# Kernel tuning notes

Hardware: AMD Instinct MI355X
Metric: run time of the kernel (lower is better)

The kernel has to match this reference:

```python
import jax, jax.numpy as jnp
import numpy as np

B, A, T, NMODE, H = 4, 16, 32, 8, 256
NSCENE = 512
HEADS = 8
FF = 128
LN_EPS = 1e-6

def _layer_norm(x, g, b, eps=LN_EPS):
    mu = jnp.mean(x, axis=-1, keepdims=True)
    var = jnp.mean((x - mu) ** 2, axis=-1, keepdims=True)
    return (x - mu) * jax.lax.rsqrt(var + eps) * g + b


def setup_inputs() -> dict:
    key = jax.random.key(0)
    ks = jax.random.split(key, 16)
    s = 1.0 / np.sqrt(H)
    sf = 1.0 / np.sqrt(FF)
    return {
        "hidden_vecs": jax.random.normal(ks[0], (B, A, T, NMODE, H), jnp.float32),
        "scene_hidden_vec": jax.random.normal(ks[1], (B, NSCENE, H), jnp.float32),
        # nn.MultiheadAttention packed in_proj: rows [Wq; Wk; Wv]
        "in_proj_w": jax.random.normal(ks[2], (3 * H, H), jnp.float32) * s,
        "in_proj_b": jnp.zeros((3 * H,), jnp.float32),
        "out_proj_w": jax.random.normal(ks[3], (H, H), jnp.float32) * s,
        "out_proj_b": jnp.zeros((H,), jnp.float32),
        "attn_ln_g": jnp.ones((H,), jnp.float32),
        "attn_ln_b": jnp.zeros((H,), jnp.float32),
        "ff1_w": jax.random.normal(ks[4], (FF, H), jnp.float32) * s,
        "ff1_b": jnp.zeros((FF,), jnp.float32),
        "ff2_w": jax.random.normal(ks[5], (H, FF), jnp.float32) * sf,
        "ff2_b": jnp.zeros((H,), jnp.float32),
        "ff_ln_g": jnp.ones((H,), jnp.float32),
        "ff_ln_b": jnp.zeros((H,), jnp.float32),
    }


def reference(hidden_vecs, scene_hidden_vec, in_proj_w, in_proj_b, out_proj_w,
              out_proj_b, attn_ln_g, attn_ln_b, ff1_w, ff1_b, ff2_w, ff2_b,
              ff_ln_g, ff_ln_b):
    b, a, t, n, h = hidden_vecs.shape
    N = scene_hidden_vec.shape[1]
    d = h // HEADS
    m = a * t * n  # queries per batch element

    Wq, Wk, Wv = in_proj_w[:h], in_proj_w[h:2 * h], in_proj_w[2 * h:]
    bq, bk, bv = in_proj_b[:h], in_proj_b[h:2 * h], in_proj_b[2 * h:]

    # Project queries; K/V computed ONCE per batch (shared across a,t,n) --
    # avoids materializing the (b,a,t,n,N,h) expanded tensor.
    q = (hidden_vecs.reshape(b, m, h) @ Wq.T + bq).reshape(b, m, HEADS, d)
    k = (scene_hidden_vec @ Wk.T + bk).reshape(b, N, HEADS, d)
    v = (scene_hidden_vec @ Wv.T + bv).reshape(b, N, HEADS, d)

    scale = 1.0 / np.sqrt(d)
    scores = jnp.einsum('bmed,bned->bemn', q * scale, k)  # (b, heads, m, N)
    attn = jax.nn.softmax(scores, axis=-1)
    ctx = jnp.einsum('bemn,bned->bmed', attn, v).reshape(b, m, h)
    attn_out = (ctx @ out_proj_w.T + out_proj_b).reshape(b, a, t, n, h)

    # averaged attention weights over heads (average_attn_weights=True)
    attn_score = jnp.mean(attn, axis=1).reshape(b, a, t, n, 1, N)

    x = _layer_norm(attn_out + hidden_vecs, attn_ln_g, attn_ln_b)
    ff = jax.nn.relu(x @ ff1_w.T + ff1_b) @ ff2_w.T + ff2_b
    out = _layer_norm(ff + x, ff_ln_g, ff_ln_b)
    return out, attn_score
```

## Files before the change

kernel.cpp:

```cpp
#include <hip/hip_runtime.h>
#include <hip/hip_bf16.h>

#define H 256
#define NSC 512
#define MQ 4096
#define BATCH 4

typedef __attribute__((ext_vector_type(8))) short bf16x8;
typedef __attribute__((ext_vector_type(4))) float f32x4;

__device__ __forceinline__ ushort f2bf(float x) {
    union { float f; unsigned u; } c; c.f = x;
    unsigned r = c.u + 0x7FFF + ((c.u >> 16) & 1);
    return (ushort)(r >> 16);
}
__device__ __forceinline__ unsigned pk2(float hi, float lo) {
    union { float f; unsigned u; } a, b; a.f = hi; b.f = lo;
    return __builtin_amdgcn_perm(a.u, b.u, 0x07060302u);
}
__device__ __forceinline__ uint4 cvt8f(const float* p) {
    float4 a = *(const float4*)p;
    float4 b = *(const float4*)(p + 4);
    uint4 r;
    r.x = pk2(a.y, a.x); r.y = pk2(a.w, a.z);
    r.z = pk2(b.y, b.x); r.w = pk2(b.w, b.z);
    return r;
}
#define EXP2(x) __builtin_amdgcn_exp2f(x)

template<int MODE>
__device__ __forceinline__ void gemm_body(
    ushort* As, ushort* Bs, int bx, int by,
    const float* __restrict__ Ain, const float* __restrict__ W,
    const float* __restrict__ bias,
    void* __restrict__ out, ushort* __restrict__ out2,
    int K, int N, float alpha)
{
    const int t = threadIdx.x;
    const int w = t >> 6, lane = t & 63, g = lane >> 4, l15 = lane & 15;
    const int rowBase = by * 64;
    const int colBase = bx * 256;
    const int wr = (w >> 2) * 32;
    const int wc = (w & 3) * 64;
    f32x4 acc[2][4];
    #pragma unroll
    for (int mt = 0; mt < 2; mt++)
        #pragma unroll
        for (int nt = 0; nt < 4; nt++) acc[mt][nt] = (f32x4){0.f,0.f,0.f,0.f};

    const int sr = t >> 3, skc = t & 7, sp = skc ^ (sr & 7);
    const size_t arow = (size_t)(rowBase + sr) * K + skc * 8;

    uint4 av = cvt8f(Ain + arow);
    uint4 bv[4];
    #pragma unroll
    for (int i = 0; i < 4; i++) {
        const int u = t + 512*i, br = u >> 3, bkc = u & 7;
        int brow = colBase + br; if (brow > N - 1) brow = N - 1;
        bv[i] = cvt8f(W + (size_t)brow * K + bkc*8);
    }

    for (int k0 = 0; k0 < K; k0 += 64) {
        __syncthreads();
        *(uint4*)&As[sr*64 + sp*8] = av;
        #pragma unroll
        for (int i = 0; i < 4; i++) {
            const int u = t + 512*i, br = u >> 3, bkc = u & 7, bp = bkc ^ (br & 7);
            *(uint4*)&Bs[br*64 + bp*8] = bv[i];
        }
        __syncthreads();
        if (k0 + 64 < K) {
            av = cvt8f(Ain + arow + k0 + 64);
            #pragma unroll
            for (int i = 0; i < 4; i++) {
                const int u = t + 512*i, br = u >> 3, bkc = u & 7;
                int brow = colBase + br; if (brow > N - 1) brow = N - 1;
                bv[i] = cvt8f(W + (size_t)brow * K + k0 + 64 + bkc*8);
            }
        }
        #pragma unroll
        for (int kk = 0; kk < 2; kk++) {
            const int swz = ((kk*4 + g) ^ (l15 & 7)) * 8;
            bf16x8 af[2], bfr[4];
            #pragma unroll
            for (int mt = 0; mt < 2; mt++)
                af[mt] = *(const bf16x8*)&As[(wr + mt*16 + l15)*64 + swz];
            #pragma unroll
            for (int nt = 0; nt < 4; nt++)
                bfr[nt] = *(const bf16x8*)&Bs[(wc + nt*16 + l15)*64 + swz];
            #pragma unroll
            for (int mt = 0; mt < 2; mt++)
                #pragma unroll
                for (int nt = 0; nt < 4; nt++)
                    acc[mt][nt] = __builtin_amdgcn_mfma_f32_16x16x32_bf16(
                        af[mt], bfr[nt], acc[mt][nt], 0, 0, 0);
        }
    }

    #pragma unroll
    for (int nt = 0; nt < 4; nt++) {
        const int col = colBase + wc + nt*16 + l15;
        const float bb = bias[col];
        #pragma unroll
        for (int mt = 0; mt < 2; mt++) {
            const int row0 = rowBase + wr + mt*16 + g*4;
            if (col < 256) {
                #pragma unroll
                for (int r = 0; r < 4; r++)
                    ((ushort*)out)[(size_t)(row0 + r) * 256 + col] = f2bf(acc[mt][nt][r] + bb);
            } else {
                ushort4 pkv = { f2bf(acc[mt][nt][0] + bb), f2bf(acc[mt][nt][1] + bb),
                                f2bf(acc[mt][nt][2] + bb), f2bf(acc[mt][nt][3] + bb) };
                *(ushort4*)&out2[(size_t)((row0 >> 9)*256 + col - 256) * 512 + (row0 & 511)] = pkv;
            }
        }
    }
}

__global__ __launch_bounds__(512, 4) void kv_kernel(
    const float* __restrict__ scene,
    const float* __restrict__ in_w, const float* __restrict__ in_b,
    ushort* __restrict__ kb, ushort* __restrict__ vtb)
{
    __shared__ ushort As[64 * 64];
    __shared__ ushort Bs[256 * 64];
    gemm_body<1>(As, Bs, blockIdx.x >> 5, blockIdx.x & 31,
                 scene, in_w + 65536, in_b + 256, kb, vtb, 256, 512, 1.f);
}

__global__ __launch_bounds__(1024, 4) void mega_kernel(
    const float* __restrict__ hidden,
    const float* __restrict__ Wq, const float* __restrict__ bq,
    const ushort* __restrict__ k, const ushort* __restrict__ vt,
    const float* __restrict__ Wo, const float* __restrict__ bo,
    const float* __restrict__ ag, const float* __restrict__ ab,
    const float* __restrict__ W1, const float* __restrict__ b1,
    const float* __restrict__ W2, const float* __restrict__ b2,
    const float* __restrict__ fg, const float* __restrict__ fbv,
    float* __restrict__ out, float* __restrict__ attn_score,
    float alpha_q)
{
    __shared__ uint4 SHraw[9120];
    ushort* SH = (ushort*)SHraw;
    ushort* Ks  = SH;
    ushort* Vs  = SH + 8448;
    ushort* Pb  = SH + 18688;
    ushort* As0 = SH;
    ushort* Bs0 = SH + 4096;
    ushort* Bs  = SH;
    ushort* Xb  = SH + 16384;
    float*  Ls  = (float*)(SH + 32768);
    float*  Lq  = (float*)(SH + 33280);
    ushort* Qb  = SH + 39168;
    ushort* Fb  = SH + 39168;
    ushort* Cb  = SH + 55552;
    float*  Lg  = (float*)(SH + 71936);

    const int t = threadIdx.x;
    const int w = t >> 6, lane = t & 63, g = lane >> 4, l15 = lane & 15;
    const int b = blockIdx.x >> 6;
    const int m0 = (blockIdx.x & 63) * 64;
    const size_t rowG = (size_t)b * MQ + m0;
    const size_t kg = (size_t)b * NSC * H;
    const size_t vg = (size_t)b * H * NSC;

    const int wr = (w >> 2) * 16;
    const int wc = (w & 3) * 64;

    {
        f32x4 acc[4];
        #pragma unroll
        for (int nt = 0; nt < 4; nt++) acc[nt] = (f32x4){0.f,0.f,0.f,0.f};

        const int sr = t >> 3, skc = t & 7, sp = skc ^ (sr & 7);
        uint4 av;
        if (t < 512) av = cvt8f(hidden + (rowG + sr) * 256 + skc*8);
        uint4 bv[2];
        #pragma unroll
        for (int i = 0; i < 2; i++) {
            const int u = t + 1024*i, br = u >> 3, bkc = u & 7;
            bv[i] = cvt8f(Wq + (size_t)br * 256 + bkc*8);
        }
        for (int k0 = 0; k0 < 256; k0 += 64) {
            __syncthreads();
            if (t < 512) *(uint4*)&As0[sr*64 + sp*8] = av;
            #pragma unroll
            for (int i = 0; i < 2; i++) {
                const int u = t + 1024*i, br = u >> 3, bkc = u & 7, bp = bkc ^ (br & 7);
                *(uint4*)&Bs0[br*64 + bp*8] = bv[i];
            }
            __syncthreads();
            if (k0 < 192) {
                if (t < 512) av = cvt8f(hidden + (rowG + sr) * 256 + k0 + 64 + skc*8);
                #pragma unroll
                for (int i = 0; i < 2; i++) {
                    const int u = t + 1024*i, br = u >> 3, bkc = u & 7;
                    bv[i] = cvt8f(Wq + (size_t)br * 256 + k0 + 64 + bkc*8);
                }
            }
            #pragma unroll
            for (int kk = 0; kk < 2; kk++) {
                const int swz = ((kk*4 + g) ^ (l15 & 7)) * 8;
                bf16x8 af = *(const bf16x8*)&As0[(wr + l15)*64 + swz];
                #pragma unroll
                for (int nt = 0; nt < 4; nt++) {
                    bf16x8 bfr = *(const bf16x8*)&Bs0[(wc + nt*16 + l15)*64 + swz];
                    acc[nt] = __builtin_amdgcn_mfma_f32_16x16x32_bf16(
                        af, bfr, acc[nt], 0, 0, 0);
                }
            }
        }
        #pragma unroll
        for (int nt = 0; nt < 4; nt++) {
            const int col = wc + nt*16 + l15;
            const float bb = bq[col];
            #pragma unroll
            for (int r = 0; r < 4; r++) {
                const int qr = wr + g*4 + r;
                const float o = (acc[nt][r] + bb) * alpha_q;
                Qb[qr*256 + (((col >> 3) ^ (qr & 7)) << 3) + (col & 7)] = f2bf(o);
            }
        }
    }
    __syncthreads();

    const int hh0 = w & 7, hf = w >> 3;
    bf16x8 qf[2];
    #pragma unroll
    for (int qt = 0; qt < 2; qt++) {
        const int qr0 = hf*32 + qt*16 + l15;
        const int c0 = hh0*32 + g*8;
        qf[qt] = *(const bf16x8*)&Qb[qr0*256 + (((c0 >> 3) ^ (qr0 & 7)) << 3)];
    }

    f32x4 cacc[2][2];
    float lacc[2][4];
    #pragma unroll
    for (int qt = 0; qt < 2; qt++) {
        #pragma unroll
        for (int dt = 0; dt < 2; dt++) cacc[qt][dt] = (f32x4){0.f,0.f,0.f,0.f};
        #pragma unroll
        for (int r = 0; r < 4; r++) lacc[qt][r] = 0.f;
    }

    const int skey = t >> 5, spart = t & 31;
    const int sd = t >> 2, sp2 = t & 3;
    bf16x8 kr = *(const bf16x8*)&k[kg + (size_t)skey*H + spart*8];
    bf16x8 vr = *(const bf16x8*)&vt[vg + (size_t)sd*NSC + sp2*8];

    for (int c = 0; c < 16; c++) {
        const int kbase = c * 32;
        __syncthreads();
        *(bf16x8*)&Ks[skey*264 + spart*8] = kr;
        *(bf16x8*)&Vs[sd*40 + sp2*8] = vr;
        __syncthreads();
        if (c < 15) {
            kr = *(const bf16x8*)&k[kg + (size_t)(kbase + 32 + skey)*H + spart*8];
            vr = *(const bf16x8*)&vt[vg + (size_t)sd*NSC + kbase + 32 + sp2*8];
        }
        #pragma unroll
        for (int qt = 0; qt < 2; qt++) {
            #pragma unroll
            for (int kt = 0; kt < 2; kt++) {
                bf16x8 kf = *(const bf16x8*)&Ks[(kt*16 + l15)*264 + hh0*32 + g*8];
                f32x4 s = __builtin_amdgcn_mfma_f32_16x16x32_bf16(
                    qf[qt], kf, (f32x4){0.f,0.f,0.f,0.f}, 0, 0, 0);
                #pragma unroll
                for (int r = 0; r < 4; r++) {
                    float p = EXP2(s[r]);
                    lacc[qt][r] += p;
                    Pb[(w*32 + qt*16 + g*4 + r)*40 + kt*16 + l15] = f2bf(p);
                }
            }
        }
        #pragma unroll
        for (int qt = 0; qt < 2; qt++) {
            bf16x8 pf = *(const bf16x8*)&Pb[(w*32 + qt*16 + l15)*40 + g*8];
            #pragma unroll
            for (int dt = 0; dt < 2; dt++) {
                bf16x8 vf = *(const bf16x8*)&Vs[(hh0*32 + dt*16 + l15)*40 + g*8];
                cacc[qt][dt] = __builtin_amdgcn_mfma_f32_16x16x32_bf16(
                    pf, vf, cacc[qt][dt], 0, 0, 0);
            }
        }
    }

    #pragma unroll
    for (int qt = 0; qt < 2; qt++) {
        float invl[4];
        #pragma unroll
        for (int r = 0; r < 4; r++) {
            float v = lacc[qt][r];
            v += __shfl_xor(v, 1); v += __shfl_xor(v, 2);
            v += __shfl_xor(v, 4); v += __shfl_xor(v, 8);
            invl[r] = 1.f / v;
            if (l15 == 0) Lg[hh0*64 + hf*32 + qt*16 + g*4 + r] = -__log2f(v) - 3.0f;
        }
        #pragma unroll
        for (int dt = 0; dt < 2; dt++)
            #pragma unroll
            for (int r = 0; r < 4; r++) {
                const int qr = hf*32 + qt*16 + g*4 + r;
                const int col = hh0*32 + dt*16 + l15;
                Cb[qr*256 + (((col >> 3) ^ (qr & 7)) << 3) + (col & 7)]
                    = f2bf(cacc[qt][dt][r] * invl[r]);
            }
    }

    __syncthreads();

    {
        f32x4 sacc[4][2];
        #pragma unroll
        for (int qt = 0; qt < 4; qt++)
            #pragma unroll
            for (int kt = 0; kt < 2; kt++) sacc[qt][kt] = (f32x4){0.f,0.f,0.f,0.f};

        #pragma unroll 2
        for (int h = 0; h < 8; h++) {
            float lgq[4]; bf16x8 qv[4];
            #pragma unroll
            for (int qt = 0; qt < 4; qt++) {
                lgq[qt] = Lg[h*64 + qt*16 + l15];
                const int qr0 = qt*16 + l15;
                const int c0 = h*32 + g*8;
                qv[qt] = *(const bf16x8*)&Qb[qr0*256 + (((c0 >> 3) ^ (qr0 & 7)) << 3)];
            }
            #pragma unroll
            for (int kt = 0; kt < 2; kt++) {
                bf16x8 kf2 = *(const bf16x8*)&k[kg + (size_t)(w*32 + kt*16 + l15)*H + h*32 + g*8];
                #pragma unroll
                for (int qt = 0; qt < 4; qt++) {
                    f32x4 s = __builtin_amdgcn_mfma_f32_16x16x32_bf16(
                        kf2, qv[qt], (f32x4){0.f,0.f,0.f,0.f}, 0, 0, 0);
                    #pragma unroll
                    for (int r = 0; r < 4; r++) sacc[qt][kt][r] += EXP2(s[r] + lgq[qt]);
                }
            }
        }
        #pragma unroll
        for (int qt = 0; qt < 4; qt++)
            #pragma unroll
            for (int kt = 0; kt < 2; kt++)
                *(f32x4*)&attn_score[(rowG + qt*16 + l15)*NSC + w*32 + kt*16 + g*4]
                    = sacc[qt][kt];
    }

    float xres[4][4];
    {
        f32x4 acc[4];
        #pragma unroll
        for (int nt = 0; nt < 4; nt++) acc[nt] = (f32x4){0.f,0.f,0.f,0.f};

        uint4 bv[2];
        #pragma unroll
        for (int i = 0; i < 2; i++) {
            const int u = t + 1024*i, br = u >> 3, bkc = u & 7;
            bv[i] = cvt8f(Wo + (size_t)br * 256 + bkc*8);
        }
        for (int k0 = 0; k0 < 256; k0 += 64) {
            __syncthreads();
            #pragma unroll
            for (int i = 0; i < 2; i++) {
                const int u = t + 1024*i, br = u >> 3, bkc = u & 7, bp = bkc ^ (br & 7);
                *(uint4*)&Bs[br*64 + bp*8] = bv[i];
            }
            __syncthreads();
            if (k0 < 192) {
                #pragma unroll
                for (int i = 0; i < 2; i++) {
                    const int u = t + 1024*i, br = u >> 3, bkc = u & 7;
                    bv[i] = cvt8f(Wo + (size_t)br * 256 + k0 + 64 + bkc*8);
                }
            }
            #pragma unroll
            for (int kk = 0; kk < 2; kk++) {
                const int rowC = wr + l15;
                const int gi = (k0 >> 3) + kk*4 + g;
                bf16x8 af = *(const bf16x8*)&Cb[rowC*256 + ((gi ^ (rowC & 7)) << 3)];
                const int swz = ((kk*4 + g) ^ (l15 & 7)) * 8;
                #pragma unroll
                for (int nt = 0; nt < 4; nt++) {
                    bf16x8 bfr = *(const bf16x8*)&Bs[(wc + nt*16 + l15)*64 + swz];
                    acc[nt] = __builtin_amdgcn_mfma_f32_16x16x32_bf16(
                        af, bfr, acc[nt], 0, 0, 0);
                }
            }
        }
        float bb[4], gmv[4], btv[4];
        #pragma unroll
        for (int nt = 0; nt < 4; nt++) {
            const int col = wc + nt*16 + l15;
            bb[nt] = bo[col]; gmv[nt] = ag[col]; btv[nt] = ab[col];
        }
        #pragma unroll
        for (int r = 0; r < 4; r++) {
            const float* rp = hidden + (rowG + wr + g*4 + r) * 256;
            #pragma unroll
            for (int nt = 0; nt < 4; nt++)
                acc[nt][r] += bb[nt] + rp[wc + nt*16 + l15];
        }
        float ps[4], pq[4];
        #pragma unroll
        for (int r = 0; r < 4; r++) {
            float s = (acc[0][r] + acc[1][r]) + (acc[2][r] + acc[3][r]);
            float qq = (acc[0][r]*acc[0][r] + acc[1][r]*acc[1][r])
                     + (acc[2][r]*acc[2][r] + acc[3][r]*acc[3][r]);
            #pragma unroll
            for (int m = 1; m < 16; m <<= 1) {
                s += __shfl_xor(s, m);
                qq += __shfl_xor(qq, m);
            }
            ps[r] = s; pq[r] = qq;
        }
        if (l15 == 0) {
            #pragma unroll
            for (int r = 0; r < 4; r++) {
                const int ri = wr + g*4 + r;
                Ls[ri*4 + (w & 3)] = ps[r];
                Lq[ri*4 + (w & 3)] = pq[r];
            }
        }
        __syncthreads();
        #pragma unroll
        for (int r = 0; r < 4; r++) {
            const int ri = wr + g*4 + r;
            f32x4 sv = *(const f32x4*)&Ls[ri*4];
            f32x4 qv2 = *(const f32x4*)&Lq[ri*4];
            const float mu = (sv[0]+sv[1]+sv[2]+sv[3]) * (1.f/256.f);
            const float ex2 = (qv2[0]+qv2[1]+qv2[2]+qv2[3]) * (1.f/256.f);
            const float rs = rsqrtf(ex2 - mu*mu + 1e-6f);
            #pragma unroll
            for (int nt = 0; nt < 4; nt++) {
                const int col = wc + nt*16 + l15;
                const float o = (acc[nt][r] - mu) * rs * gmv[nt] + btv[nt];
                xres[nt][r] = o;
                Xb[ri*256 + (((col >> 3) ^ (ri & 7)) << 3) + (col & 7)] = f2bf(o);
            }
        }
    }

    {
        const int wrB = (w >> 2) * 16;
        const int wcB = (w & 3) * 32;
        f32x4 facc[2];
        #pragma unroll
        for (int nt = 0; nt < 2; nt++) facc[nt] = (f32x4){0.f,0.f,0.f,0.f};

        uint4 bv2 = cvt8f(W1 + (size_t)(t >> 3) * 256 + (t & 7)*8);
        for (int k0 = 0; k0 < 256; k0 += 64) {
            __syncthreads();
            {
                const int br = t >> 3, bkc = t & 7, bp = bkc ^ (br & 7);
                *(uint4*)&Bs[br*64 + bp*8] = bv2;
            }
            __syncthreads();
            if (k0 < 192)
                bv2 = cvt8f(W1 + (size_t)(t >> 3) * 256 + k0 + 64 + (t & 7)*8);
            #pragma unroll
            for (int kk = 0; kk < 2; kk++) {
                const int rowX = wrB + l15;
                const int gi = (k0 >> 3) + kk*4 + g;
                bf16x8 af = *(const bf16x8*)&Xb[rowX*256 + ((gi ^ (rowX & 7)) << 3)];
                const int swz = ((kk*4 + g) ^ (l15 & 7)) * 8;
                #pragma unroll
                for (int nt = 0; nt < 2; nt++) {
                    bf16x8 bfr = *(const bf16x8*)&Bs[(wcB + nt*16 + l15)*64 + swz];
                    facc[nt] = __builtin_amdgcn_mfma_f32_16x16x32_bf16(
                        af, bfr, facc[nt], 0, 0, 0);
                }
            }
        }
        __syncthreads();
        #pragma unroll
        for (int nt = 0; nt < 2; nt++) {
            const int colF = wcB + nt*16 + l15;
            const float fbb = b1[colF];
            #pragma unroll
            for (int r = 0; r < 4; r++) {
                const int rowF = wrB + g*4 + r;
                const float o = fmaxf(facc[nt][r] + fbb, 0.f);
                Fb[rowF*128 + (((colF >> 3) ^ (rowF & 7)) << 3) + (colF & 7)] = f2bf(o);
            }
        }
        __syncthreads();
    }

    {
        f32x4 acc2[4];
        #pragma unroll
        for (int nt = 0; nt < 4; nt++) acc2[nt] = (f32x4){0.f,0.f,0.f,0.f};

        uint4 bv3[2];
        #pragma unroll
        for (int i = 0; i < 2; i++) {
            const int u = t + 1024*i, br = u >> 3, bkc = u & 7;
            bv3[i] = cvt8f(W2 + (size_t)br * 128 + bkc*8);
        }
        for (int k0 = 0; k0 < 128; k0 += 64) {
            __syncthreads();
            #pragma unroll
            for (int i = 0; i < 2; i++) {
                const int u = t + 1024*i, br = u >> 3, bkc = u & 7, bp = bkc ^ (br & 7);
                *(uint4*)&Bs[br*64 + bp*8] = bv3[i];
            }
            __syncthreads();
            if (k0 == 0) {
                #pragma unroll
                for (int i = 0; i < 2; i++) {
                    const int u = t + 1024*i, br = u >> 3, bkc = u & 7;
                    bv3[i] = cvt8f(W2 + (size_t)br * 128 + 64 + bkc*8);
                }
            }
            #pragma unroll
            for (int kk = 0; kk < 2; kk++) {
                const int gi = (k0 >> 3) + kk*4 + g;
                const int rowF = wr + l15;
                bf16x8 af2 = *(const bf16x8*)&Fb[rowF*128 + ((gi ^ (rowF & 7)) << 3)];
                const int swz = ((kk*4 + g) ^ (l15 & 7)) * 8;
                #pragma unroll
                for (int nt = 0; nt < 4; nt++) {
                    bf16x8 bfr = *(const bf16x8*)&Bs[(wc + nt*16 + l15)*64 + swz];
                    acc2[nt] = __builtin_amdgcn_mfma_f32_16x16x32_bf16(
                        af2, bfr, acc2[nt], 0, 0, 0);
                }
            }
        }
        float bb[4], gmv[4], btv[4];
        #pragma unroll
        for (int nt = 0; nt < 4; nt++) {
            const int col = wc + nt*16 + l15;
            bb[nt] = b2[col]; gmv[nt] = fg[col]; btv[nt] = fbv[col];
        }
        #pragma unroll
        for (int r = 0; r < 4; r++)
            #pragma unroll
            for (int nt = 0; nt < 4; nt++)
                acc2[nt][r] += bb[nt] + xres[nt][r];
        float ps[4], pq[4];
        #pragma unroll
        for (int r = 0; r < 4; r++) {
            float s = (acc2[0][r] + acc2[1][r]) + (acc2[2][r] + acc2[3][r]);
            float qq = (acc2[0][r]*acc2[0][r] + acc2[1][r]*acc2[1][r])
                     + (acc2[2][r]*acc2[2][r] + acc2[3][r]*acc2[3][r]);
            #pragma unroll
            for (int m = 1; m < 16; m <<= 1) {
                s += __shfl_xor(s, m);
                qq += __shfl_xor(qq, m);
            }
            ps[r] = s; pq[r] = qq;
        }
        __syncthreads();
        if (l15 == 0) {
            #pragma unroll
            for (int r = 0; r < 4; r++) {
                const int ri = wr + g*4 + r;
                Ls[ri*4 + (w & 3)] = ps[r];
                Lq[ri*4 + (w & 3)] = pq[r];
            }
        }
        __syncthreads();
        #pragma unroll
        for (int r = 0; r < 4; r++) {
            const int ri = wr + g*4 + r;
            f32x4 sv = *(const f32x4*)&Ls[ri*4];
            f32x4 qv2 = *(const f32x4*)&Lq[ri*4];
            const float mu = (sv[0]+sv[1]+sv[2]+sv[3]) * (1.f/256.f);
            const float ex2 = (qv2[0]+qv2[1]+qv2[2]+qv2[3]) * (1.f/256.f);
            const float rs = rsqrtf(ex2 - mu*mu + 1e-6f);
            #pragma unroll
            for (int nt = 0; nt < 4; nt++) {
                const int col = wc + nt*16 + l15;
                out[(rowG + ri) * 256 + col] =
                    (acc2[nt][r] - mu) * rs * gmv[nt] + btv[nt];
            }
        }
    }
}

extern "C" void kernel_launch(void* const* d_in, const int* in_sizes, int n_in,
                              void* d_out, int out_size, void* d_ws, size_t ws_size,
                              hipStream_t stream)
{
    const float* hidden = (const float*)d_in[0];
    const float* scene  = (const float*)d_in[1];
    const float* in_w   = (const float*)d_in[2];
    const float* in_b   = (const float*)d_in[3];
    const float* out_w  = (const float*)d_in[4];
    const float* out_b  = (const float*)d_in[5];
    const float* aln_g  = (const float*)d_in[6];
    const float* aln_b  = (const float*)d_in[7];
    const float* ff1_w  = (const float*)d_in[8];
    const float* ff1_b  = (const float*)d_in[9];
    const float* ff2_w  = (const float*)d_in[10];
    const float* ff2_b  = (const float*)d_in[11];
    const float* fln_g  = (const float*)d_in[12];
    const float* fln_b  = (const float*)d_in[13];

    float* out0  = (float*)d_out;
    float* score = out0 + (size_t)BATCH * MQ * H;

    ushort* kb   = (ushort*)d_ws;
    ushort* vtb  = kb + 524288;

    const float alpha_q = 0.25507609683638066f;

    kv_kernel<<<dim3(64), dim3(512), 0, stream>>>(scene, in_w, in_b, kb, vtb);
    mega_kernel<<<dim3(256), dim3(1024), 0, stream>>>(
        hidden, in_w, in_b, kb, vtb,
        out_w, out_b, aln_g, aln_b,
        ff1_w, ff1_b, ff2_w, ff2_b, fln_g, fln_b,
        out0, score, alpha_q);
}
```

Baseline: 167.2 us.

## Halve mega_kernel query tile to 32 rows with 512 threads

Each block of the fused attention+FFN kernel now handles 32 query rows with 8 waves instead of 64 rows with 16 waves, and the grid doubles to 512 blocks. The LDS layout is shrunk and remapped, and each wave now owns one head across all 32 queries. Per-wave P staging is merged into the QK loop, and V fragments are hoisted out of the loop. This is meant to give more blocks than the 256 CUs to fill the GPU and to cut LDS per block for higher occupancy. The cost is that K/V and weight tiles are reloaded twice as many times in total.

```diff
diff --git a/kernel.cpp b/kernel.cpp
--- a/kernel.cpp
+++ b/kernel.cpp
@@ -128,7 +128,7 @@
                  scene, in_w + 65536, in_b + 256, kb, vtb, 256, 512, 1.f);
 }
 
-__global__ __launch_bounds__(1024, 4) void mega_kernel(
+__global__ __launch_bounds__(512, 4) void mega_kernel(
     const float* __restrict__ hidden,
     const float* __restrict__ Wq, const float* __restrict__ bq,
     const ushort* __restrict__ k, const ushort* __restrict__ vt,
@@ -140,26 +140,26 @@
     float* __restrict__ out, float* __restrict__ attn_score,
     float alpha_q)
 {
-    __shared__ uint4 SHraw[9120];
+    __shared__ uint4 SHraw[5088];
     ushort* SH = (ushort*)SHraw;
     ushort* Ks  = SH;
     ushort* Vs  = SH + 8448;
     ushort* Pb  = SH + 18688;
     ushort* As0 = SH;
-    ushort* Bs0 = SH + 4096;
+    ushort* Bs0 = SH + 2048;
     ushort* Bs  = SH;
-    ushort* Xb  = SH + 16384;
-    float*  Ls  = (float*)(SH + 32768);
-    float*  Lq  = (float*)(SH + 33280);
-    ushort* Qb  = SH + 39168;
-    ushort* Fb  = SH + 39168;
-    ushort* Cb  = SH + 55552;
-    float*  Lg  = (float*)(SH + 71936);
+    float*  Ls  = (float*)(SH + 16384);
+    float*  Lq  = (float*)(SH + 16640);
+    ushort* Qb  = SH + 23808;
+    ushort* Xb  = SH + 23808;
+    ushort* Cb  = SH + 32000;
+    ushort* Fb  = SH + 32000;
+    float*  Lg  = (float*)(SH + 40192);
 
     const int t = threadIdx.x;
     const int w = t >> 6, lane = t & 63, g = lane >> 4, l15 = lane & 15;
-    const int b = blockIdx.x >> 6;
-    const int m0 = (blockIdx.x & 63) * 64;
+    const int b = blockIdx.x >> 7;
+    const int m0 = (blockIdx.x & 127) * 32;
     const size_t rowG = (size_t)b * MQ + m0;
     const size_t kg = (size_t)b * NSC * H;
     const size_t vg = (size_t)b * H * NSC;
@@ -174,27 +174,27 @@
 
         const int sr = t >> 3, skc = t & 7, sp = skc ^ (sr & 7);
         uint4 av;
-        if (t < 512) av = cvt8f(hidden + (rowG + sr) * 256 + skc*8);
-        uint4 bv[2];
-        #pragma unroll
-        for (int i = 0; i < 2; i++) {
-            const int u = t + 1024*i, br = u >> 3, bkc = u & 7;
+        if (t < 256) av = cvt8f(hidden + (rowG + sr) * 256 + skc*8);
+        uint4 bv[4];
+        #pragma unroll
+        for (int i = 0; i < 4; i++) {
+            const int u = t + 512*i, br = u >> 3, bkc = u & 7;
             bv[i] = cvt8f(Wq + (size_t)br * 256 + bkc*8);
         }
         for (int k0 = 0; k0 < 256; k0 += 64) {
             __syncthreads();
-            if (t < 512) *(uint4*)&As0[sr*64 + sp*8] = av;
-            #pragma unroll
-            for (int i = 0; i < 2; i++) {
-                const int u = t + 1024*i, br = u >> 3, bkc = u & 7, bp = bkc ^ (br & 7);
+            if (t < 256) *(uint4*)&As0[sr*64 + sp*8] = av;
+            #pragma unroll
+            for (int i = 0; i < 4; i++) {
+                const int u = t + 512*i, br = u >> 3, bkc = u & 7, bp = bkc ^ (br & 7);
                 *(uint4*)&Bs0[br*64 + bp*8] = bv[i];
             }
             __syncthreads();
             if (k0 < 192) {
-                if (t < 512) av = cvt8f(hidden + (rowG + sr) * 256 + k0 + 64 + skc*8);
-                #pragma unroll
-                for (int i = 0; i < 2; i++) {
-                    const int u = t + 1024*i, br = u >> 3, bkc = u & 7;
+                if (t < 256) av = cvt8f(hidden + (rowG + sr) * 256 + k0 + 64 + skc*8);
+                #pragma unroll
+                for (int i = 0; i < 4; i++) {
+                    const int u = t + 512*i, br = u >> 3, bkc = u & 7;
                     bv[i] = cvt8f(Wq + (size_t)br * 256 + k0 + 64 + bkc*8);
                 }
             }
@@ -224,13 +224,11 @@
     }
     __syncthreads();
 
-    const int hh0 = w & 7, hf = w >> 3;
     bf16x8 qf[2];
     #pragma unroll
     for (int qt = 0; qt < 2; qt++) {
-        const int qr0 = hf*32 + qt*16 + l15;
-        const int c0 = hh0*32 + g*8;
-        qf[qt] = *(const bf16x8*)&Qb[qr0*256 + (((c0 >> 3) ^ (qr0 & 7)) << 3)];
+        const int qr0 = qt*16 + l15;
+        qf[qt] = *(const bf16x8*)&Qb[qr0*256 + (((w*4 + g) ^ (qr0 & 7)) << 3)];
     }
 
     f32x4 cacc[2][2];
@@ -243,45 +241,56 @@
         for (int r = 0; r < 4; r++) lacc[qt][r] = 0.f;
     }
 
-    const int skey = t >> 5, spart = t & 31;
-    const int sd = t >> 2, sp2 = t & 3;
-    bf16x8 kr = *(const bf16x8*)&k[kg + (size_t)skey*H + spart*8];
-    bf16x8 vr = *(const bf16x8*)&vt[vg + (size_t)sd*NSC + sp2*8];
+    bf16x8 kr[2], vr[2];
+    #pragma unroll
+    for (int i = 0; i < 2; i++) {
+        const int u = t + 512*i;
+        kr[i] = *(const bf16x8*)&k[kg + (size_t)(u >> 5)*H + (u & 31)*8];
+        vr[i] = *(const bf16x8*)&vt[vg + (size_t)(u >> 2)*NSC + (u & 3)*8];
+    }
+    ushort* PbW = Pb + w*640;
 
     for (int c = 0; c < 16; c++) {
         const int kbase = c * 32;
         __syncthreads();
-        *(bf16x8*)&Ks[skey*264 + spart*8] = kr;
-        *(bf16x8*)&Vs[sd*40 + sp2*8] = vr;
+        #pragma unroll
+        for (int i = 0; i < 2; i++) {
+            const int u = t + 512*i;
+            *(bf16x8*)&Ks[(u >> 5)*264 + (u & 31)*8] = kr[i];
+            *(bf16x8*)&Vs[(u >> 2)*40 + (u & 3)*8] = vr[i];
+        }
         __syncthreads();
         if (c < 15) {
-            kr = *(const bf16x8*)&k[kg + (size_t)(kbase + 32 + skey)*H + spart*8];
-            vr = *(const bf16x8*)&vt[vg + (size_t)sd*NSC + kbase + 32 + sp2*8];
-        }
+            #pragma unroll
+            for (int i = 0; i < 2; i++) {
+                const int u = t + 512*i;
+                kr[i] = *(const bf16x8*)&k[kg + (size_t)(kbase + 32 + (u >> 5))*H + (u & 31)*8];
+                vr[i] = *(const bf16x8*)&vt[vg + (size_t)(u >> 2)*NSC + kbase + 32 + (u & 3)*8];
+            }
+        }
+        bf16x8 vfv[2];
+        #pragma unroll
+        for (int dt = 0; dt < 2; dt++)
+            vfv[dt] = *(const bf16x8*)&Vs[(w*32 + dt*16 + l15)*40 + g*8];
         #pragma unroll
         for (int qt = 0; qt < 2; qt++) {
             #pragma unroll
             for (int kt = 0; kt < 2; kt++) {
-                bf16x8 kf = *(const bf16x8*)&Ks[(kt*16 + l15)*264 + hh0*32 + g*8];
+                bf16x8 kf = *(const bf16x8*)&Ks[(kt*16 + l15)*264 + w*32 + g*8];
                 f32x4 s = __builtin_amdgcn_mfma_f32_16x16x32_bf16(
                     qf[qt], kf, (f32x4){0.f,0.f,0.f,0.f}, 0, 0, 0);
                 #pragma unroll
                 for (int r = 0; r < 4; r++) {
                     float p = EXP2(s[r]);
                     lacc[qt][r] += p;
-                    Pb[(w*32 + qt*16 + g*4 + r)*40 + kt*16 + l15] = f2bf(p);
-                }
-            }
-        }
-        #pragma unroll
-        for (int qt = 0; qt < 2; qt++) {
-            bf16x8 pf = *(const bf16x8*)&Pb[(w*32 + qt*16 + l15)*40 + g*8];
-            #pragma unroll
-            for (int dt = 0; dt < 2; dt++) {
-                bf16x8 vf = *(const bf16x8*)&Vs[(hh0*32 + dt*16 + l15)*40 + g*8];
+                    PbW[(g*4 + r)*40 + kt*16 + l15] = f2bf(p);
+                }
+            }
+            bf16x8 pf = *(const bf16x8*)&PbW[l15*40 + g*8];
+            #pragma unroll
+            for (int dt = 0; dt < 2; dt++)
                 cacc[qt][dt] = __builtin_amdgcn_mfma_f32_16x16x32_bf16(
-                    pf, vf, cacc[qt][dt], 0, 0, 0);
-            }
+                    pf, vfv[dt], cacc[qt][dt], 0, 0, 0);
         }
     }
 
@@ -294,14 +303,14 @@
             v += __shfl_xor(v, 1); v += __shfl_xor(v, 2);
             v += __shfl_xor(v, 4); v += __shfl_xor(v, 8);
             invl[r] = 1.f / v;
-            if (l15 == 0) Lg[hh0*64 + hf*32 + qt*16 + g*4 + r] = -__log2f(v) - 3.0f;
+            if (l15 == 0) Lg[w*32 + qt*16 + g*4 + r] = -__log2f(v) - 3.0f;
         }
         #pragma unroll
         for (int dt = 0; dt < 2; dt++)
             #pragma unroll
             for (int r = 0; r < 4; r++) {
-                const int qr = hf*32 + qt*16 + g*4 + r;
-                const int col = hh0*32 + dt*16 + l15;
+                const int qr = qt*16 + g*4 + r;
+                const int col = w*32 + dt*16 + l15;
                 Cb[qr*256 + (((col >> 3) ^ (qr & 7)) << 3) + (col & 7)]
                     = f2bf(cacc[qt][dt][r] * invl[r]);
             }
@@ -310,39 +319,36 @@
     __syncthreads();
 
     {
-        f32x4 sacc[4][2];
-        #pragma unroll
-        for (int qt = 0; qt < 4; qt++)
-            #pragma unroll
-            for (int kt = 0; kt < 2; kt++) sacc[qt][kt] = (f32x4){0.f,0.f,0.f,0.f};
+        f32x4 sacc[2][4];
+        #pragma unroll
+        for (int qt = 0; qt < 2; qt++)
+            #pragma unroll
+            for (int kt = 0; kt < 4; kt++) sacc[qt][kt] = (f32x4){0.f,0.f,0.f,0.f};
 
         #pragma unroll 2
         for (int h = 0; h < 8; h++) {
-            float lgq[4]; bf16x8 qv[4];
-            #pragma unroll
-            for (int qt = 0; qt < 4; qt++) {
-                lgq[qt] = Lg[h*64 + qt*16 + l15];
-                const int qr0 = qt*16 + l15;
-                const int c0 = h*32 + g*8;
-                qv[qt] = *(const bf16x8*)&Qb[qr0*256 + (((c0 >> 3) ^ (qr0 & 7)) << 3)];
-            }
-            #pragma unroll
-            for (int kt = 0; kt < 2; kt++) {
-                bf16x8 kf2 = *(const bf16x8*)&k[kg + (size_t)(w*32 + kt*16 + l15)*H + h*32 + g*8];
-                #pragma unroll
-                for (int qt = 0; qt < 4; qt++) {
-                    f32x4 s = __builtin_amdgcn_mfma_f32_16x16x32_bf16(
-                        kf2, qv[qt], (f32x4){0.f,0.f,0.f,0.f}, 0, 0, 0);
-                    #pragma unroll
-                    for (int r = 0; r < 4; r++) sacc[qt][kt][r] += EXP2(s[r] + lgq[qt]);
-                }
-            }
-        }
-        #pragma unroll
-        for (int qt = 0; qt < 4; qt++)
-            #pragma unroll
-            for (int kt = 0; kt < 2; kt++)
-                *(f32x4*)&attn_score[(rowG + qt*16 + l15)*NSC + w*32 + kt*16 + g*4]
+            const float lg0 = Lg[h*32 + l15];
+            const float lg1 = Lg[h*32 + 16 + l15];
+            bf16x8 q0 = *(const bf16x8*)&Qb[l15*256 + (((h*4 + g) ^ (l15 & 7)) << 3)];
+            bf16x8 q1 = *(const bf16x8*)&Qb[(16 + l15)*256 + (((h*4 + g) ^ (l15 & 7)) << 3)];
+            #pragma unroll
+            for (int kt = 0; kt < 4; kt++) {
+                bf16x8 kf2 = *(const bf16x8*)&k[kg + (size_t)(w*64 + kt*16 + l15)*H + h*32 + g*8];
+                f32x4 s0 = __builtin_amdgcn_mfma_f32_16x16x32_bf16(
+                    kf2, q0, (f32x4){0.f,0.f,0.f,0.f}, 0, 0, 0);
+                #pragma unroll
+                for (int r = 0; r < 4; r++) sacc[0][kt][r] += EXP2(s0[r] + lg0);
+                f32x4 s1 = __builtin_amdgcn_mfma_f32_16x16x32_bf16(
+                    kf2, q1, (f32x4){0.f,0.f,0.f,0.f}, 0, 0, 0);
+                #pragma unroll
+                for (int r = 0; r < 4; r++) sacc[1][kt][r] += EXP2(s1[r] + lg1);
+            }
+        }
+        #pragma unroll
+        for (int qt = 0; qt < 2; qt++)
+            #pragma unroll
+            for (int kt = 0; kt < 4; kt++)
+                *(f32x4*)&attn_score[(rowG + qt*16 + l15)*NSC + w*64 + kt*16 + g*4]
                     = sacc[qt][kt];
     }
 
@@ -352,24 +358,24 @@
         #pragma unroll
         for (int nt = 0; nt < 4; nt++) acc[nt] = (f32x4){0.f,0.f,0.f,0.f};
 
-        uint4 bv[2];
-        #pragma unroll
-        for (int i = 0; i < 2; i++) {
-            const int u = t + 1024*i, br = u >> 3, bkc = u & 7;
+        uint4 bv[4];
+        #pragma unroll
+        for (int i = 0; i < 4; i++) {
+            const int u = t + 512*i, br = u >> 3, bkc = u & 7;
             bv[i] = cvt8f(Wo + (size_t)br * 256 + bkc*8);
         }
         for (int k0 = 0; k0 < 256; k0 += 64) {
             __syncthreads();
             #pragma unroll
-            for (int i = 0; i < 2; i++) {
-                const int u = t + 1024*i, br = u >> 3, bkc = u & 7, bp = bkc ^ (br & 7);
+            for (int i = 0; i < 4; i++) {
+                const int u = t + 512*i, br = u >> 3, bkc = u & 7, bp = bkc ^ (br & 7);
                 *(uint4*)&Bs[br*64 + bp*8] = bv[i];
             }
             __syncthreads();
             if (k0 < 192) {
                 #pragma unroll
-                for (int i = 0; i < 2; i++) {
-                    const int u = t + 1024*i, br = u >> 3, bkc = u & 7;
+                for (int i = 0; i < 4; i++) {
+                    const int u = t + 512*i, br = u >> 3, bkc = u & 7;
                     bv[i] = cvt8f(Wo + (size_t)br * 256 + k0 + 64 + bkc*8);
                 }
             }
@@ -447,16 +453,27 @@
         #pragma unroll
         for (int nt = 0; nt < 2; nt++) facc[nt] = (f32x4){0.f,0.f,0.f,0.f};
 
-        uint4 bv2 = cvt8f(W1 + (size_t)(t >> 3) * 256 + (t & 7)*8);
+        uint4 bv2[2];
+        #pragma unroll
+        for (int i = 0; i < 2; i++) {
+            const int u = t + 512*i, br = u >> 3, bkc = u & 7;
+            bv2[i] = cvt8f(W1 + (size_t)br * 256 + bkc*8);
+        }
         for (int k0 = 0; k0 < 256; k0 += 64) {
             __syncthreads();
-            {
-                const int br = t >> 3, bkc = t & 7, bp = bkc ^ (br & 7);
-                *(uint4*)&Bs[br*64 + bp*8] = bv2;
-            }
-            __syncthreads();
-            if (k0 < 192)
-                bv2 = cvt8f(W1 + (size_t)(t >> 3) * 256 + k0 + 64 + (t & 7)*8);
+            #pragma unroll
+            for (int i = 0; i < 2; i++) {
+                const int u = t + 512*i, br = u >> 3, bkc = u & 7, bp = bkc ^ (br & 7);
+                *(uint4*)&Bs[br*64 + bp*8] = bv2[i];
+            }
+            __syncthreads();
+            if (k0 < 192) {
+                #pragma unroll
+                for (int i = 0; i < 2; i++) {
+                    const int u = t + 512*i, br = u >> 3, bkc = u & 7;
+                    bv2[i] = cvt8f(W1 + (size_t)br * 256 + k0 + 64 + bkc*8);
+                }
+            }
             #pragma unroll
             for (int kk = 0; kk < 2; kk++) {
                 const int rowX = wrB + l15;
@@ -491,24 +508,24 @@
         #pragma unroll
         for (int nt = 0; nt < 4; nt++) acc2[nt] = (f32x4){0.f,0.f,0.f,0.f};
 
-        uint4 bv3[2];
-        #pragma unroll
-        for (int i = 0; i < 2; i++) {
-            const int u = t + 1024*i, br = u >> 3, bkc = u & 7;
+        uint4 bv3[4];
+        #pragma unroll
+        for (int i = 0; i < 4; i++) {
+            const int u = t + 512*i, br = u >> 3, bkc = u & 7;
             bv3[i] = cvt8f(W2 + (size_t)br * 128 + bkc*8);
         }
         for (int k0 = 0; k0 < 128; k0 += 64) {
             __syncthreads();
             #pragma unroll
-            for (int i = 0; i < 2; i++) {
-                const int u = t + 1024*i, br = u >> 3, bkc = u & 7, bp = bkc ^ (br & 7);
+            for (int i = 0; i < 4; i++) {
+                const int u = t + 512*i, br = u >> 3, bkc = u & 7, bp = bkc ^ (br & 7);
                 *(uint4*)&Bs[br*64 + bp*8] = bv3[i];
             }
             __syncthreads();
             if (k0 == 0) {
                 #pragma unroll
-                for (int i = 0; i < 2; i++) {
-                    const int u = t + 1024*i, br = u >> 3, bkc = u & 7;
+                for (int i = 0; i < 4; i++) {
+                    const int u = t + 512*i, br = u >> 3, bkc = u & 7;
                     bv3[i] = cvt8f(W2 + (size_t)br * 128 + 64 + bkc*8);
                 }
             }
@@ -606,7 +623,7 @@
     const float alpha_q = 0.25507609683638066f;
 
     kv_kernel<<<dim3(64), dim3(512), 0, stream>>>(scene, in_w, in_b, kb, vtb);
-    mega_kernel<<<dim3(256), dim3(1024), 0, stream>>>(
+    mega_kernel<<<dim3(512), dim3(512), 0, stream>>>(
         hidden, in_w, in_b, kb, vtb,
         out_w, out_b, aln_g, aln_b,
         ff1_w, ff1_b, ff2_w, ff2_b, fln_g, fln_b,
```

Result: slower. 175.1 us (+4.7%).

## Double K-step tile depth in fused attention and GEMM stages, prefetch K/V early

Applied to the files above, without the earlier changes.

Raises the K-dimension staging chunk from 64 to 128 in the Q-projection, out-projection, FF1 and FF2 GEMMs, and from 32 to 64 keys per attention chunk. This halves the number of barrier-separated load/compute iterations. The shared-memory layout is reorganised, with XOR swizzles replacing the padded strides for K/V. The first K/V chunk is also prefetched before the Q projection so its latency overlaps that GEMM. The cost is more shared memory and more registers per thread, which could lower occupancy or cause spills.

```diff
diff --git a/kernel.cpp b/kernel.cpp
--- a/kernel.cpp
+++ b/kernel.cpp
@@ -140,21 +140,21 @@
     float* __restrict__ out, float* __restrict__ attn_score,
     float alpha_q)
 {
-    __shared__ uint4 SHraw[9120];
+    __shared__ uint4 SHraw[9600];
     ushort* SH = (ushort*)SHraw;
     ushort* Ks  = SH;
-    ushort* Vs  = SH + 8448;
-    ushort* Pb  = SH + 18688;
+    ushort* Vs  = SH + 16384;
+    ushort* Pb  = SH + 32768;
     ushort* As0 = SH;
-    ushort* Bs0 = SH + 4096;
+    ushort* Bs0 = SH + 8192;
     ushort* Bs  = SH;
-    ushort* Xb  = SH + 16384;
     float*  Ls  = (float*)(SH + 32768);
     float*  Lq  = (float*)(SH + 33280);
-    ushort* Qb  = SH + 39168;
-    ushort* Fb  = SH + 39168;
-    ushort* Cb  = SH + 55552;
-    float*  Lg  = (float*)(SH + 71936);
+    ushort* Qb  = SH + 43008;
+    ushort* Xb  = SH + 43008;
+    ushort* Cb  = SH + 59392;
+    ushort* Fb  = SH + 59392;
+    float*  Lg  = (float*)(SH + 75776);
 
     const int t = threadIdx.x;
     const int w = t >> 6, lane = t & 63, g = lane >> 4, l15 = lane & 15;
@@ -167,44 +167,51 @@
     const int wr = (w >> 2) * 16;
     const int wc = (w & 3) * 64;
 
+    bf16x8 kr[2], vr[2];
+    #pragma unroll
+    for (int i = 0; i < 2; i++) {
+        const int u = t + 1024*i;
+        kr[i] = *(const bf16x8*)&k[kg + (size_t)(u >> 5)*H + (u & 31)*8];
+        vr[i] = *(const bf16x8*)&vt[vg + (size_t)(u >> 3)*NSC + (u & 7)*8];
+    }
+
     {
         f32x4 acc[4];
         #pragma unroll
         for (int nt = 0; nt < 4; nt++) acc[nt] = (f32x4){0.f,0.f,0.f,0.f};
 
-        const int sr = t >> 3, skc = t & 7, sp = skc ^ (sr & 7);
-        uint4 av;
-        if (t < 512) av = cvt8f(hidden + (rowG + sr) * 256 + skc*8);
-        uint4 bv[2];
-        #pragma unroll
-        for (int i = 0; i < 2; i++) {
-            const int u = t + 1024*i, br = u >> 3, bkc = u & 7;
-            bv[i] = cvt8f(Wq + (size_t)br * 256 + bkc*8);
-        }
-        for (int k0 = 0; k0 < 256; k0 += 64) {
+        const int ar = t >> 4, agi = t & 15;
+        uint4 av = cvt8f(hidden + (rowG + ar) * 256 + agi*8);
+        uint4 bv[4];
+        #pragma unroll
+        for (int i = 0; i < 4; i++) {
+            const int u = t + 1024*i, br = u >> 4, bgi = u & 15;
+            bv[i] = cvt8f(Wq + (size_t)br * 256 + bgi*8);
+        }
+        for (int k0 = 0; k0 < 256; k0 += 128) {
             __syncthreads();
-            if (t < 512) *(uint4*)&As0[sr*64 + sp*8] = av;
-            #pragma unroll
-            for (int i = 0; i < 2; i++) {
-                const int u = t + 1024*i, br = u >> 3, bkc = u & 7, bp = bkc ^ (br & 7);
-                *(uint4*)&Bs0[br*64 + bp*8] = bv[i];
+            *(uint4*)&As0[ar*128 + ((agi ^ (ar & 7)))*8] = av;
+            #pragma unroll
+            for (int i = 0; i < 4; i++) {
+                const int u = t + 1024*i, br = u >> 4, bgi = u & 15;
+                *(uint4*)&Bs0[br*128 + ((bgi ^ (br & 7)))*8] = bv[i];
             }
             __syncthreads();
-            if (k0 < 192) {
-                if (t < 512) av = cvt8f(hidden + (rowG + sr) * 256 + k0 + 64 + skc*8);
-                #pragma unroll
-                for (int i = 0; i < 2; i++) {
-                    const int u = t + 1024*i, br = u >> 3, bkc = u & 7;
-                    bv[i] = cvt8f(Wq + (size_t)br * 256 + k0 + 64 + bkc*8);
-                }
-            }
-            #pragma unroll
-            for (int kk = 0; kk < 2; kk++) {
+            if (k0 == 0) {
+                av = cvt8f(hidden + (rowG + ar) * 256 + 128 + agi*8);
+                #pragma unroll
+                for (int i = 0; i < 4; i++) {
+                    const int u = t + 1024*i, br = u >> 4, bgi = u & 15;
+                    bv[i] = cvt8f(Wq + (size_t)br * 256 + 128 + bgi*8);
+                }
+            }
+            #pragma unroll
+            for (int kk = 0; kk < 4; kk++) {
                 const int swz = ((kk*4 + g) ^ (l15 & 7)) * 8;
-                bf16x8 af = *(const bf16x8*)&As0[(wr + l15)*64 + swz];
+                bf16x8 af = *(const bf16x8*)&As0[(wr + l15)*128 + swz];
                 #pragma unroll
                 for (int nt = 0; nt < 4; nt++) {
-                    bf16x8 bfr = *(const bf16x8*)&Bs0[(wc + nt*16 + l15)*64 + swz];
+                    bf16x8 bfr = *(const bf16x8*)&Bs0[(wc + nt*16 + l15)*128 + swz];
                     acc[nt] = __builtin_amdgcn_mfma_f32_16x16x32_bf16(
                         af, bfr, acc[nt], 0, 0, 0);
                 }
@@ -229,8 +236,7 @@
     #pragma unroll
     for (int qt = 0; qt < 2; qt++) {
         const int qr0 = hf*32 + qt*16 + l15;
-        const int c0 = hh0*32 + g*8;
-        qf[qt] = *(const bf16x8*)&Qb[qr0*256 + (((c0 >> 3) ^ (qr0 & 7)) << 3)];
+        qf[qt] = *(const bf16x8*)&Qb[qr0*256 + (((hh0*4 + g) ^ (qr0 & 7)) << 3)];
     }
 
     f32x4 cacc[2][2];
@@ -242,45 +248,56 @@
         #pragma unroll
         for (int r = 0; r < 4; r++) lacc[qt][r] = 0.f;
     }
-
-    const int skey = t >> 5, spart = t & 31;
-    const int sd = t >> 2, sp2 = t & 3;
-    bf16x8 kr = *(const bf16x8*)&k[kg + (size_t)skey*H + spart*8];
-    bf16x8 vr = *(const bf16x8*)&vt[vg + (size_t)sd*NSC + sp2*8];
-
-    for (int c = 0; c < 16; c++) {
-        const int kbase = c * 32;
-        __syncthreads();
-        *(bf16x8*)&Ks[skey*264 + spart*8] = kr;
-        *(bf16x8*)&Vs[sd*40 + sp2*8] = vr;
-        __syncthreads();
-        if (c < 15) {
-            kr = *(const bf16x8*)&k[kg + (size_t)(kbase + 32 + skey)*H + spart*8];
-            vr = *(const bf16x8*)&vt[vg + (size_t)sd*NSC + kbase + 32 + sp2*8];
-        }
-        #pragma unroll
-        for (int qt = 0; qt < 2; qt++) {
-            #pragma unroll
-            for (int kt = 0; kt < 2; kt++) {
-                bf16x8 kf = *(const bf16x8*)&Ks[(kt*16 + l15)*264 + hh0*32 + g*8];
-                f32x4 s = __builtin_amdgcn_mfma_f32_16x16x32_bf16(
-                    qf[qt], kf, (f32x4){0.f,0.f,0.f,0.f}, 0, 0, 0);
-                #pragma unroll
-                for (int r = 0; r < 4; r++) {
-                    float p = EXP2(s[r]);
-                    lacc[qt][r] += p;
-                    Pb[(w*32 + qt*16 + g*4 + r)*40 + kt*16 + l15] = f2bf(p);
-                }
-            }
-        }
-        #pragma unroll
-        for (int qt = 0; qt < 2; qt++) {
-            bf16x8 pf = *(const bf16x8*)&Pb[(w*32 + qt*16 + l15)*40 + g*8];
+    ushort* PbW = Pb + w*640;
+
+    for (int c = 0; c < 8; c++) {
+        const int kbase = c * 64;
+        __syncthreads();
+        #pragma unroll
+        for (int i = 0; i < 2; i++) {
+            const int u = t + 1024*i;
+            const int key = u >> 5, gi = u & 31;
+            *(bf16x8*)&Ks[key*256 + ((gi ^ (key & 7)))*8] = kr[i];
+            const int d = u >> 3, gj = u & 7;
+            *(bf16x8*)&Vs[d*64 + ((gj ^ (d & 7)))*8] = vr[i];
+        }
+        __syncthreads();
+        if (c < 7) {
+            #pragma unroll
+            for (int i = 0; i < 2; i++) {
+                const int u = t + 1024*i;
+                kr[i] = *(const bf16x8*)&k[kg + (size_t)(kbase + 64 + (u >> 5))*H + (u & 31)*8];
+                vr[i] = *(const bf16x8*)&vt[vg + (size_t)(u >> 3)*NSC + kbase + 64 + (u & 7)*8];
+            }
+        }
+        #pragma unroll
+        for (int ks2 = 0; ks2 < 2; ks2++) {
+            bf16x8 vfv[2];
             #pragma unroll
             for (int dt = 0; dt < 2; dt++) {
-                bf16x8 vf = *(const bf16x8*)&Vs[(hh0*32 + dt*16 + l15)*40 + g*8];
-                cacc[qt][dt] = __builtin_amdgcn_mfma_f32_16x16x32_bf16(
-                    pf, vf, cacc[qt][dt], 0, 0, 0);
+                const int d = hh0*32 + dt*16 + l15;
+                vfv[dt] = *(const bf16x8*)&Vs[d*64 + (((ks2*4 + g) ^ (l15 & 7)) << 3)];
+            }
+            #pragma unroll
+            for (int qt = 0; qt < 2; qt++) {
+                #pragma unroll
+                for (int kt = 0; kt < 2; kt++) {
+                    const int key = ks2*32 + kt*16 + l15;
+                    bf16x8 kf = *(const bf16x8*)&Ks[key*256 + (((hh0*4 + g) ^ (l15 & 7)) << 3)];
+                    f32x4 s = __builtin_amdgcn_mfma_f32_16x16x32_bf16(
+                        qf[qt], kf, (f32x4){0.f,0.f,0.f,0.f}, 0, 0, 0);
+                    #pragma unroll
+                    for (int r = 0; r < 4; r++) {
+                        float p = EXP2(s[r]);
+                        lacc[qt][r] += p;
+                        PbW[(g*4 + r)*40 + kt*16 + l15] = f2bf(p);
+                    }
+                }
+                bf16x8 pf = *(const bf16x8*)&PbW[l15*40 + g*8];
+                #pragma unroll
+                for (int dt = 0; dt < 2; dt++)
+                    cacc[qt][dt] = __builtin_amdgcn_mfma_f32_16x16x32_bf16(
+                        pf, vfv[dt], cacc[qt][dt], 0, 0, 0);
             }
         }
     }
@@ -323,8 +340,7 @@
             for (int qt = 0; qt < 4; qt++) {
                 lgq[qt] = Lg[h*64 + qt*16 + l15];
                 const int qr0 = qt*16 + l15;
-                const int c0 = h*32 + g*8;
-                qv[qt] = *(const bf16x8*)&Qb[qr0*256 + (((c0 >> 3) ^ (qr0 & 7)) << 3)];
+                qv[qt] = *(const bf16x8*)&Qb[qr0*256 + (((h*4 + g) ^ (qr0 & 7)) << 3)];
             }
             #pragma unroll
             for (int kt = 0; kt < 2; kt++) {
@@ -352,36 +368,36 @@
         #pragma unroll
         for (int nt = 0; nt < 4; nt++) acc[nt] = (f32x4){0.f,0.f,0.f,0.f};
 
-        uint4 bv[2];
-        #pragma unroll
-        for (int i = 0; i < 2; i++) {
-            const int u = t + 1024*i, br = u >> 3, bkc = u & 7;
-            bv[i] = cvt8f(Wo + (size_t)br * 256 + bkc*8);
-        }
-        for (int k0 = 0; k0 < 256; k0 += 64) {
+        uint4 bv[4];
+        #pragma unroll
+        for (int i = 0; i < 4; i++) {
+            const int u = t + 1024*i, br = u >> 4, bgi = u & 15;
+            bv[i] = cvt8f(Wo + (size_t)br * 256 + bgi*8);
+        }
+        for (int k0 = 0; k0 < 256; k0 += 128) {
             __syncthreads();
             #pragma unroll
-            for (int i = 0; i < 2; i++) {
-                const int u = t + 1024*i, br = u >> 3, bkc = u & 7, bp = bkc ^ (br & 7);
-                *(uint4*)&Bs[br*64 + bp*8] = bv[i];
+            for (int i = 0; i < 4; i++) {
+                const int u = t + 1024*i, br = u >> 4, bgi = u & 15;
+                *(uint4*)&Bs[br*128 + ((bgi ^ (br & 7)))*8] = bv[i];
             }
             __syncthreads();
-            if (k0 < 192) {
-                #pragma unroll
-                for (int i = 0; i < 2; i++) {
-                    const int u = t + 1024*i, br = u >> 3, bkc = u & 7;
-                    bv[i] = cvt8f(Wo + (size_t)br * 256 + k0 + 64 + bkc*8);
-                }
-            }
-            #pragma unroll
-            for (int kk = 0; kk < 2; kk++) {
+            if (k0 == 0) {
+                #pragma unroll
+                for (int i = 0; i < 4; i++) {
+                    const int u = t + 1024*i, br = u >> 4, bgi = u & 15;
+                    bv[i] = cvt8f(Wo + (size_t)br * 256 + 128 + bgi*8);
+                }
+            }
+            #pragma unroll
+            for (int kk = 0; kk < 4; kk++) {
                 const int rowC = wr + l15;
                 const int gi = (k0 >> 3) + kk*4 + g;
                 bf16x8 af = *(const bf16x8*)&Cb[rowC*256 + ((gi ^ (rowC & 7)) << 3)];
                 const int swz = ((kk*4 + g) ^ (l15 & 7)) * 8;
                 #pragma unroll
                 for (int nt = 0; nt < 4; nt++) {
-                    bf16x8 bfr = *(const bf16x8*)&Bs[(wc + nt*16 + l15)*64 + swz];
+                    bf16x8 bfr = *(const bf16x8*)&Bs[(wc + nt*16 + l15)*128 + swz];
                     acc[nt] = __builtin_amdgcn_mfma_f32_16x16x32_bf16(
                         af, bfr, acc[nt], 0, 0, 0);
                 }
@@ -447,25 +463,36 @@
         #pragma unroll
         for (int nt = 0; nt < 2; nt++) facc[nt] = (f32x4){0.f,0.f,0.f,0.f};
 
-        uint4 bv2 = cvt8f(W1 + (size_t)(t >> 3) * 256 + (t & 7)*8);
-        for (int k0 = 0; k0 < 256; k0 += 64) {
+        uint4 bv2[2];
+        #pragma unroll
+        for (int i = 0; i < 2; i++) {
+            const int u = t + 1024*i, br = u >> 4, bgi = u & 15;
+            bv2[i] = cvt8f(W1 + (size_t)br * 256 + bgi*8);
+        }
+        for (int k0 = 0; k0 < 256; k0 += 128) {
             __syncthreads();
-            {
-                const int br = t >> 3, bkc = t & 7, bp = bkc ^ (br & 7);
-                *(uint4*)&Bs[br*64 + bp*8] = bv2;
+            #pragma unroll
+            for (int i = 0; i < 2; i++) {
+                const int u = t + 1024*i, br = u >> 4, bgi = u & 15;
+                *(uint4*)&Bs[br*128 + ((bgi ^ (br & 7)))*8] = bv2[i];
             }
             __syncthreads();
-            if (k0 < 192)
-                bv2 = cvt8f(W1 + (size_t)(t >> 3) * 256 + k0 + 64 + (t & 7)*8);
-            #pragma unroll
-            for (int kk = 0; kk < 2; kk++) {
+            if (k0 == 0) {
+                #pragma unroll
+                for (int i = 0; i < 2; i++) {
+                    const int u = t + 1024*i, br = u >> 4, bgi = u & 15;
+                    bv2[i] = cvt8f(W1 + (size_t)br * 256 + 128 + bgi*8);
+                }
+            }
+            #pragma unroll
+            for (int kk = 0; kk < 4; kk++) {
                 const int rowX = wrB + l15;
                 const int gi = (k0 >> 3) + kk*4 + g;
                 bf16x8 af = *(const bf16x8*)&Xb[rowX*256 + ((gi ^ (rowX & 7)) << 3)];
                 const int swz = ((kk*4 + g) ^ (l15 & 7)) * 8;
                 #pragma unroll
                 for (int nt = 0; nt < 2; nt++) {
-                    bf16x8 bfr = *(const bf16x8*)&Bs[(wcB + nt*16 + l15)*64 + swz];
+                    bf16x8 bfr = *(const bf16x8*)&Bs[(wcB + nt*16 + l15)*128 + swz];
                     facc[nt] = __builtin_amdgcn_mfma_f32_16x16x32_bf16(
                         af, bfr, facc[nt], 0, 0, 0);
                 }
@@ -491,39 +518,30 @@
         #pragma unroll
         for (int nt = 0; nt < 4; nt++) acc2[nt] = (f32x4){0.f,0.f,0.f,0.f};
 
-        uint4 bv3[2];
-        #pragma unroll
-        for (int i = 0; i < 2; i++) {
-            const int u = t + 1024*i, br = u >> 3, bkc = u & 7;
-            bv3[i] = cvt8f(W2 + (size_t)br * 128 + bkc*8);
-        }
-        for (int k0 = 0; k0 < 128; k0 += 64) {
-            __syncthreads();
-            #pragma unroll
-            for (int i = 0; i < 2; i++) {
-                const int u = t + 1024*i, br = u >> 3, bkc = u & 7, bp = bkc ^ (br & 7);
-                *(uint4*)&Bs[br*64 + bp*8] = bv3[i];
-            }
-            __syncthreads();
-            if (k0 == 0) {
-                #pragma unroll
-                for (int i = 0; i < 2; i++) {
-                    const int u = t + 1024*i, br = u >> 3, bkc = u & 7;
-                    bv3[i] = cvt8f(W2 + (size_t)br * 128 + 64 + bkc*8);
-                }
-            }
-            #pragma unroll
-            for (int kk = 0; kk < 2; kk++) {
-                const int gi = (k0 >> 3) + kk*4 + g;
-                const int rowF = wr + l15;
-                bf16x8 af2 = *(const bf16x8*)&Fb[rowF*128 + ((gi ^ (rowF & 7)) << 3)];
-                const int swz = ((kk*4 + g) ^ (l15 & 7)) * 8;
-                #pragma unroll
-                for (int nt = 0; nt < 4; nt++) {
-                    bf16x8 bfr = *(const bf16x8*)&Bs[(wc + nt*16 + l15)*64 + swz];
-                    acc2[nt] = __builtin_amdgcn_mfma_f32_16x16x32_bf16(
-                        af2, bfr, acc2[nt], 0, 0, 0);
-                }
+        uint4 bv3[4];
+        #pragma unroll
+        for (int i = 0; i < 4; i++) {
+            const int u = t + 1024*i, br = u >> 4, bgi = u & 15;
+            bv3[i] = cvt8f(W2 + (size_t)br * 128 + bgi*8);
+        }
+        __syncthreads();
+        #pragma unroll
+        for (int i = 0; i < 4; i++) {
+            const int u = t + 1024*i, br = u >> 4, bgi = u & 15;
+            *(uint4*)&Bs[br*128 + ((bgi ^ (br & 7)))*8] = bv3[i];
+        }
+        __syncthreads();
+        #pragma unroll
+        for (int kk = 0; kk < 4; kk++) {
+            const int gi = kk*4 + g;
+            const int rowF = wr + l15;
+            bf16x8 af2 = *(const bf16x8*)&Fb[rowF*128 + ((gi ^ (rowF & 7)) << 3)];
+            const int swz = (gi ^ (l15 & 7)) * 8;
+            #pragma unroll
+            for (int nt = 0; nt < 4; nt++) {
+                bf16x8 bfr = *(const bf16x8*)&Bs[(wc + nt*16 + l15)*128 + swz];
+                acc2[nt] = __builtin_amdgcn_mfma_f32_16x16x32_bf16(
+                    af2, bfr, acc2[nt], 0, 0, 0);
             }
         }
         float bb[4], gmv[4], btv[4];
```

After: 179.8 us. 1.08x slower.
